# Kernel tuning notes

Hardware: AMD Instinct MI355X
Metric: run time of the kernel (lower is better)

The kernel has to match this reference:

```python
import jax, jax.numpy as jnp
import numpy as np

TOP_K = 8


def setup_inputs() -> dict:
    key = jax.random.key(0)
    k1, k2, k3 = jax.random.split(key, 3)
    N, D, SQRT_K = 8192, 2048, 64
    x = jax.random.normal(k1, (N, D), dtype=jnp.float32)
    W1 = jax.random.normal(k2, (SQRT_K, D), dtype=jnp.float32) * (1.0 / np.sqrt(D))
    W2 = jax.random.normal(k3, (SQRT_K, D), dtype=jnp.float32) * (1.0 / np.sqrt(D))
    return {"x": x, "W1": W1, "W2": W2}


def reference(x, W1, W2):
    # Two small projections: [N, d] @ [d, sqrt_K] -> [N, sqrt_K]
    s1 = jnp.einsum('nd,kd->nk', x, W1)
    s2 = jnp.einsum('nd,kd->nk', x, W2)
    # Outer-sum score matrix: expert (i, j) scores s1[i] + s2[j]; flatten -> [N, sqrt_K^2]
    scores = (s1[:, :, None] + s2[:, None, :]).reshape(x.shape[0], -1)
    topk_vals, topk_idx = jax.lax.top_k(scores, TOP_K)
    probs = jax.nn.softmax(topk_vals, axis=-1)
    return topk_idx, probs, scores
```

## Files before the change

### kernel.cpp

```cpp
#include <hip/hip_runtime.h>
#include <math.h>

#define NROWS 8192
#define DDIM  2048
#define NEXP  4096
#define TK    8
#define KSPLIT 4
#define KRANGE (DDIM / KSPLIT)
#define BM     64

typedef float  f4 __attribute__((ext_vector_type(4)));
typedef double d2 __attribute__((ext_vector_type(2)));

__global__ __launch_bounds__(256, 2) void pkr_gemm64w(const float* __restrict__ x,
                                                      const float* __restrict__ w1,
                                                      const float* __restrict__ w2,
                                                      float* __restrict__ out) {
  __shared__ double xsd[32][66];
  __shared__ double wsd[32][130];

  const int tid   = threadIdx.x;
  const int rb    = blockIdx.x >> 2;
  const int kp    = blockIdx.x & 3;
  const int rows0 = rb * BM;
  const int kbase = kp * KRANGE;

  const int rh = tid >> 4;
  const int ch = tid & 15;

  const int sxr = tid >> 3;
  const int sxk = (tid & 7) * 4;
  const float* xr0 = x + (size_t)(rows0 + sxr) * DDIM + kbase + sxk;
  const float* xr1 = xr0 + (size_t)32 * DDIM;

  const int swc = tid >> 1;
  const int swk = (tid & 1) * 16;
  const float* wr = ((swc < 64) ? (w1 + (size_t)swc * DDIM)
                                : (w2 + (size_t)(swc - 64) * DDIM)) + kbase + swk;

  double acc[4][8] = {};

  for (int cch = 0; cch < KRANGE / 32; ++cch) {
    const int k0 = cch * 32;
    {
      f4 a = *(const f4*)(xr0 + k0);
      f4 b = *(const f4*)(xr1 + k0);
#pragma unroll
      for (int q = 0; q < 4; ++q) {
        xsd[sxk + q][sxr]      = (double)a[q];
        xsd[sxk + q][32 + sxr] = (double)b[q];
      }
    }
#pragma unroll
    for (int p = 0; p < 4; ++p) {
      f4 wv = *(const f4*)(wr + k0 + p * 4);
#pragma unroll
      for (int q = 0; q < 4; ++q)
        wsd[swk + p * 4 + q][swc] = (double)wv[q];
    }
    __syncthreads();

#pragma unroll
    for (int k = 0; k < 32; ++k) {
      const d2 x01 = *(const d2*)&xsd[k][rh * 4];
      const d2 x23 = *(const d2*)&xsd[k][rh * 4 + 2];
      const double xd[4] = { x01[0], x01[1], x23[0], x23[1] };
      d2 wg[4];
#pragma unroll
      for (int g = 0; g < 4; ++g) wg[g] = *(const d2*)&wsd[k][g * 32 + ch * 2];
#pragma unroll
      for (int a = 0; a < 4; ++a)
#pragma unroll
        for (int g = 0; g < 4; ++g) {
          acc[a][2 * g]     += xd[a] * wg[g][0];
          acc[a][2 * g + 1] += xd[a] * wg[g][1];
        }
    }
    __syncthreads();
  }

  double* P = (double*)(out + (size_t)2 * NROWS * TK);
#pragma unroll
  for (int a = 0; a < 4; ++a) {
    double* dst = P + (size_t)(rows0 + rh * 4 + a) * (NEXP / 2) + kp * 128;
#pragma unroll
    for (int g = 0; g < 4; ++g) {
      d2 v; v[0] = acc[a][2 * g]; v[1] = acc[a][2 * g + 1];
      *(d2*)(dst + g * 32 + ch * 2) = v;
    }
  }
}

__device__ __forceinline__ void bitonic64(double& v, int& idx, int lane) {
#pragma unroll
  for (int k = 2; k <= 64; k <<= 1) {
#pragma unroll
    for (int j = k >> 1; j > 0; j >>= 1) {
      const double ov = __shfl_xor(v, j);
      const int    oi = __shfl_xor(idx, j);
      const bool obetter = (ov > v) || (ov == v && oi < idx);
      const bool lower   = (lane & j) == 0;
      const bool up      = (lane & k) == 0;
      if ((lower == up) ? obetter : !obetter) { v = ov; idx = oi; }
    }
  }
}

__global__ __launch_bounds__(256) void pkr_finish(float* __restrict__ out) {
  const int lane = threadIdx.x & 63;
  const int wv   = threadIdx.x >> 6;
  const int row  = blockIdx.x * 4 + wv;

  const double* Pr = (const double*)(out + (size_t)2 * NROWS * TK) + (size_t)row * (NEXP / 2);
  double s1 = 0.0, s2 = 0.0;
#pragma unroll
  for (int p = 0; p < KSPLIT; ++p) {
    s1 += Pr[p * 128 + lane];
    s2 += Pr[p * 128 + 64 + lane];
  }

  __shared__ double sh1[4][64], sh2[4][64];
  sh1[wv][lane] = s1;
  sh2[wv][lane] = s2;
  __syncthreads();

  {
    float* srow = out + (size_t)2 * NROWS * TK + (size_t)row * NEXP;
    const int il = lane >> 4;
    const int jq = (lane & 15) * 4;
    const double sj0 = sh2[wv][jq + 0], sj1 = sh2[wv][jq + 1];
    const double sj2 = sh2[wv][jq + 2], sj3 = sh2[wv][jq + 3];
#pragma unroll
    for (int i0 = 0; i0 < 64; i0 += 4) {
      const double si = sh1[wv][i0 + il];
      f4 v;
      v[0] = (float)(si + sj0);
      v[1] = (float)(si + sj1);
      v[2] = (float)(si + sj2);
      v[3] = (float)(si + sj3);
      *(f4*)(srow + (size_t)(i0 + il) * 64 + jq) = v;
    }
  }

  double v1 = s1; int i1 = lane;
  bitonic64(v1, i1, lane);
  double v2 = s2; int i2 = lane;
  bitonic64(v2, i2, lane);

  const double ca = __shfl(v1, lane >> 3);
  const int    ia = __shfl(i1, lane >> 3);
  const double cb = __shfl(v2, lane & 7);
  const int    ib = __shfl(i2, lane & 7);
  double cv = ca + cb;
  int    ci = ia * 64 + ib;
  bitonic64(cv, ci, lane);

  const double vmax = __shfl(cv, 0);
  float e = expf((float)(cv - vmax));
  float sum = e;
#pragma unroll
  for (int off = 1; off < 8; off <<= 1) sum += __shfl_xor(sum, off);
  if (lane < 8) {
    out[(size_t)row * TK + lane]                      = (float)ci;
    out[(size_t)NROWS * TK + (size_t)row * TK + lane] = e / sum;
  }
}

extern "C" void kernel_launch(void* const* d_in, const int* in_sizes, int n_in,
                              void* d_out, int out_size, void* d_ws, size_t ws_size,
                              hipStream_t stream) {
  const float* x  = (const float*)d_in[0];
  const float* w1 = (const float*)d_in[1];
  const float* w2 = (const float*)d_in[2];
  float* out = (float*)d_out;

  hipLaunchKernelGGL(pkr_gemm64w, dim3((NROWS / BM) * KSPLIT), dim3(256), 0, stream,
                     x, w1, w2, out);
  hipLaunchKernelGGL(pkr_finish, dim3(NROWS / 4), dim3(256), 0, stream, out);
}
```

Measured before the change: 273.9 us.

## Enlarge GEMM tile to 128 rows, prefetch via registers, split top-k into per-thread kernel

The GEMM now covers 128 rows per block with an 8x8 fp64 accumulator per thread. x is staged in LDS as fp32 and converted on read, and the next chunk is prefetched into registers while the current one computes. Top-k selection moves to a separate kernel where each thread handles one row with serial insertion into sorted lists, replacing the wave-level bitonic sorts, and score expansion becomes its own third kernel. This trades more registers, lower occupancy and an extra launch for more data reuse per LDS load, and the top-k kernel launches only 128 blocks of 64 threads.

```diff
diff --git a/kernel.cpp b/kernel.cpp
--- a/kernel.cpp
+++ b/kernel.cpp
@@ -7,17 +7,22 @@
 #define TK    8
 #define KSPLIT 4
 #define KRANGE (DDIM / KSPLIT)
-#define BM     64
+#define BM     128
+#define BK     32
+#define NCH    (KRANGE / BK)
+#define XS     162
+#define WS     162
 
 typedef float  f4 __attribute__((ext_vector_type(4)));
+typedef float  f2 __attribute__((ext_vector_type(2)));
 typedef double d2 __attribute__((ext_vector_type(2)));
 
-__global__ __launch_bounds__(256, 2) void pkr_gemm64w(const float* __restrict__ x,
-                                                      const float* __restrict__ w1,
-                                                      const float* __restrict__ w2,
-                                                      float* __restrict__ out) {
-  __shared__ double xsd[32][66];
-  __shared__ double wsd[32][130];
+__global__ __launch_bounds__(256) void pkr_gemm(const float* __restrict__ x,
+                                                const float* __restrict__ w1,
+                                                const float* __restrict__ w2,
+                                                float* __restrict__ out) {
+  __shared__ float  xs[BK][XS];
+  __shared__ double wsd[BK][WS];
 
   const int tid   = threadIdx.x;
   const int rb    = blockIdx.x >> 2;
@@ -25,88 +30,148 @@
   const int rows0 = rb * BM;
   const int kbase = kp * KRANGE;
 
-  const int rh = tid >> 4;
-  const int ch = tid & 15;
-
-  const int sxr = tid >> 3;
-  const int sxk = (tid & 7) * 4;
-  const float* xr0 = x + (size_t)(rows0 + sxr) * DDIM + kbase + sxk;
-  const float* xr1 = xr0 + (size_t)32 * DDIM;
-
-  const int swc = tid >> 1;
-  const int swk = (tid & 1) * 16;
-  const float* wr = ((swc < 64) ? (w1 + (size_t)swc * DDIM)
-                                : (w2 + (size_t)(swc - 64) * DDIM)) + kbase + swk;
-
-  double acc[4][8] = {};
-
-  for (int cch = 0; cch < KRANGE / 32; ++cch) {
-    const int k0 = cch * 32;
-    {
-      f4 a = *(const f4*)(xr0 + k0);
-      f4 b = *(const f4*)(xr1 + k0);
+  const int tr   = tid >> 4;
+  const int tc   = tid & 15;
+  const int tr10 = tr * 10;
+  const int tc10 = tc * 10;
+
+  int mp[4], mk[4];
+  const float* xp[4];
+  const float* wp[4];
+#pragma unroll
+  for (int i = 0; i < 4; ++i) {
+    const int s  = i * 256 + tid;
+    const int r  = s >> 3;
+    const int kq = (s & 7) * 4;
+    mp[i] = r + (r >> 3) * 2;
+    mk[i] = kq;
+    xp[i] = x + (size_t)(rows0 + r) * DDIM + kbase + kq;
+    wp[i] = ((r < 64) ? (w1 + (size_t)r * DDIM)
+                      : (w2 + (size_t)(r - 64) * DDIM)) + kbase + kq;
+  }
+
+  f4 xfr[4], wfr[4];
+
+  auto load_regs = [&](int ch) {
+    const int o = ch * BK;
+#pragma unroll
+    for (int i = 0; i < 4; ++i) {
+      xfr[i] = *(const f4*)(xp[i] + o);
+      wfr[i] = *(const f4*)(wp[i] + o);
+    }
+  };
+  auto write_lds = [&]() {
+#pragma unroll
+    for (int i = 0; i < 4; ++i)
 #pragma unroll
       for (int q = 0; q < 4; ++q) {
-        xsd[sxk + q][sxr]      = (double)a[q];
-        xsd[sxk + q][32 + sxr] = (double)b[q];
+        xs[mk[i] + q][mp[i]]  = xfr[i][q];
+        wsd[mk[i] + q][mp[i]] = (double)wfr[i][q];
       }
-    }
-#pragma unroll
-    for (int p = 0; p < 4; ++p) {
-      f4 wv = *(const f4*)(wr + k0 + p * 4);
-#pragma unroll
-      for (int q = 0; q < 4; ++q)
-        wsd[swk + p * 4 + q][swc] = (double)wv[q];
+  };
+
+  double acc[8][8] = {};
+
+  load_regs(0);
+  write_lds();
+  __syncthreads();
+
+  for (int ch = 0; ch < NCH; ++ch) {
+    if (ch + 1 < NCH) load_regs(ch + 1);
+#pragma unroll 4
+    for (int k = 0; k < BK; ++k) {
+      double xd[8];
+      d2 wd[4];
+#pragma unroll
+      for (int m = 0; m < 4; ++m) {
+        const f2 xv = *(const f2*)&xs[k][tr10 + 2 * m];
+        xd[2 * m]     = (double)xv[0];
+        xd[2 * m + 1] = (double)xv[1];
+        wd[m] = *(const d2*)&wsd[k][tc10 + 2 * m];
+      }
+#pragma unroll
+      for (int a = 0; a < 8; ++a)
+#pragma unroll
+        for (int m = 0; m < 4; ++m) {
+          acc[a][2 * m]     += xd[a] * wd[m][0];
+          acc[a][2 * m + 1] += xd[a] * wd[m][1];
+        }
     }
     __syncthreads();
-
-#pragma unroll
-    for (int k = 0; k < 32; ++k) {
-      const d2 x01 = *(const d2*)&xsd[k][rh * 4];
-      const d2 x23 = *(const d2*)&xsd[k][rh * 4 + 2];
-      const double xd[4] = { x01[0], x01[1], x23[0], x23[1] };
-      d2 wg[4];
-#pragma unroll
-      for (int g = 0; g < 4; ++g) wg[g] = *(const d2*)&wsd[k][g * 32 + ch * 2];
-#pragma unroll
-      for (int a = 0; a < 4; ++a)
-#pragma unroll
-        for (int g = 0; g < 4; ++g) {
-          acc[a][2 * g]     += xd[a] * wg[g][0];
-          acc[a][2 * g + 1] += xd[a] * wg[g][1];
-        }
-    }
-    __syncthreads();
+    if (ch + 1 < NCH) {
+      write_lds();
+      __syncthreads();
+    }
   }
 
   double* P = (double*)(out + (size_t)2 * NROWS * TK);
 #pragma unroll
-  for (int a = 0; a < 4; ++a) {
-    double* dst = P + (size_t)(rows0 + rh * 4 + a) * (NEXP / 2) + kp * 128;
-#pragma unroll
-    for (int g = 0; g < 4; ++g) {
-      d2 v; v[0] = acc[a][2 * g]; v[1] = acc[a][2 * g + 1];
-      *(d2*)(dst + g * 32 + ch * 2) = v;
-    }
-  }
-}
-
-__device__ __forceinline__ void bitonic64(double& v, int& idx, int lane) {
-#pragma unroll
-  for (int k = 2; k <= 64; k <<= 1) {
-#pragma unroll
-    for (int j = k >> 1; j > 0; j >>= 1) {
-      const double ov = __shfl_xor(v, j);
-      const int    oi = __shfl_xor(idx, j);
-      const bool obetter = (ov > v) || (ov == v && oi < idx);
-      const bool lower   = (lane & j) == 0;
-      const bool up      = (lane & k) == 0;
-      if ((lower == up) ? obetter : !obetter) { v = ov; idx = oi; }
-    }
-  }
-}
-
-__global__ __launch_bounds__(256) void pkr_finish(float* __restrict__ out) {
+  for (int a = 0; a < 8; ++a) {
+    double* dst = P + (size_t)(rows0 + tr * 8 + a) * (NEXP / 2) + kp * 128 + tc * 8;
+#pragma unroll
+    for (int m = 0; m < 4; ++m) {
+      d2 v; v[0] = acc[a][2 * m]; v[1] = acc[a][2 * m + 1];
+      *(d2*)(dst + 2 * m) = v;
+    }
+  }
+}
+
+__device__ __forceinline__ void ins8(double v, int i, double* av, int* ai) {
+  bool b[8];
+#pragma unroll
+  for (int j = 0; j < 8; ++j)
+    b[j] = (v > av[j]) || (v == av[j] && i < ai[j]);
+#pragma unroll
+  for (int j = 7; j > 0; --j) {
+    av[j] = b[j] ? (b[j - 1] ? av[j - 1] : v) : av[j];
+    ai[j] = b[j] ? (b[j - 1] ? ai[j - 1] : i) : ai[j];
+  }
+  if (b[0]) { av[0] = v; ai[0] = i; }
+}
+
+__global__ __launch_bounds__(64) void pkr_topk(float* __restrict__ out) {
+  const int row = blockIdx.x * 64 + threadIdx.x;
+  const double* Pr = (const double*)(out + (size_t)2 * NROWS * TK) + (size_t)row * (NEXP / 2);
+
+  double av[8], bv[8], cv[8];
+  int    ai[8], bi[8], ci[8];
+#pragma unroll
+  for (int t = 0; t < 8; ++t) {
+    av[t] = bv[t] = cv[t] = -INFINITY;
+    ai[t] = bi[t] = ci[t] = 0x7fffffff;
+  }
+
+  for (int j = 0; j < 64; ++j) {
+    const double s = Pr[j] + Pr[128 + j] + Pr[256 + j] + Pr[384 + j];
+    ins8(s, j, av, ai);
+  }
+  for (int j = 0; j < 64; ++j) {
+    const double s = Pr[64 + j] + Pr[192 + j] + Pr[320 + j] + Pr[448 + j];
+    ins8(s, j, bv, bi);
+  }
+#pragma unroll
+  for (int p = 0; p < 8; ++p)
+#pragma unroll
+    for (int q = 0; q < 8; ++q)
+      ins8(av[p] + bv[q], ai[p] * 64 + bi[q], cv, ci);
+
+  float e[8], sum = 0.f;
+#pragma unroll
+  for (int t = 0; t < 8; ++t) { e[t] = expf((float)(cv[t] - cv[0])); sum += e[t]; }
+  const float inv = 1.0f / sum;
+  f4 vi0, vi1, vp0, vp1;
+#pragma unroll
+  for (int t = 0; t < 4; ++t) {
+    vi0[t] = (float)ci[t];     vi1[t] = (float)ci[t + 4];
+    vp0[t] = e[t] * inv;       vp1[t] = e[t + 4] * inv;
+  }
+  float* oi = out + (size_t)row * TK;
+  float* op = out + (size_t)NROWS * TK + (size_t)row * TK;
+  *(f4*)oi = vi0; *(f4*)(oi + 4) = vi1;
+  *(f4*)op = vp0; *(f4*)(op + 4) = vp1;
+}
+
+__global__ __launch_bounds__(256) void pkr_expand(float* __restrict__ out) {
   const int lane = threadIdx.x & 63;
   const int wv   = threadIdx.x >> 6;
   const int row  = blockIdx.x * 4 + wv;
@@ -124,45 +189,20 @@
   sh2[wv][lane] = s2;
   __syncthreads();
 
-  {
-    float* srow = out + (size_t)2 * NROWS * TK + (size_t)row * NEXP;
-    const int il = lane >> 4;
-    const int jq = (lane & 15) * 4;
-    const double sj0 = sh2[wv][jq + 0], sj1 = sh2[wv][jq + 1];
-    const double sj2 = sh2[wv][jq + 2], sj3 = sh2[wv][jq + 3];
-#pragma unroll
-    for (int i0 = 0; i0 < 64; i0 += 4) {
-      const double si = sh1[wv][i0 + il];
-      f4 v;
-      v[0] = (float)(si + sj0);
-      v[1] = (float)(si + sj1);
-      v[2] = (float)(si + sj2);
-      v[3] = (float)(si + sj3);
-      *(f4*)(srow + (size_t)(i0 + il) * 64 + jq) = v;
-    }
-  }
-
-  double v1 = s1; int i1 = lane;
-  bitonic64(v1, i1, lane);
-  double v2 = s2; int i2 = lane;
-  bitonic64(v2, i2, lane);
-
-  const double ca = __shfl(v1, lane >> 3);
-  const int    ia = __shfl(i1, lane >> 3);
-  const double cb = __shfl(v2, lane & 7);
-  const int    ib = __shfl(i2, lane & 7);
-  double cv = ca + cb;
-  int    ci = ia * 64 + ib;
-  bitonic64(cv, ci, lane);
-
-  const double vmax = __shfl(cv, 0);
-  float e = expf((float)(cv - vmax));
-  float sum = e;
-#pragma unroll
-  for (int off = 1; off < 8; off <<= 1) sum += __shfl_xor(sum, off);
-  if (lane < 8) {
-    out[(size_t)row * TK + lane]                      = (float)ci;
-    out[(size_t)NROWS * TK + (size_t)row * TK + lane] = e / sum;
+  float* srow = out + (size_t)2 * NROWS * TK + (size_t)row * NEXP;
+  const int il = lane >> 4;
+  const int jq = (lane & 15) * 4;
+  const double sj0 = sh2[wv][jq + 0], sj1 = sh2[wv][jq + 1];
+  const double sj2 = sh2[wv][jq + 2], sj3 = sh2[wv][jq + 3];
+#pragma unroll
+  for (int i0 = 0; i0 < 64; i0 += 4) {
+    const double si = sh1[wv][i0 + il];
+    f4 v;
+    v[0] = (float)(si + sj0);
+    v[1] = (float)(si + sj1);
+    v[2] = (float)(si + sj2);
+    v[3] = (float)(si + sj3);
+    *(f4*)(srow + (size_t)(i0 + il) * 64 + jq) = v;
   }
 }
 
@@ -174,7 +214,8 @@
   const float* w2 = (const float*)d_in[2];
   float* out = (float*)d_out;
 
-  hipLaunchKernelGGL(pkr_gemm64w, dim3((NROWS / BM) * KSPLIT), dim3(256), 0, stream,
+  hipLaunchKernelGGL(pkr_gemm, dim3((NROWS / BM) * KSPLIT), dim3(256), 0, stream,
                      x, w1, w2, out);
-  hipLaunchKernelGGL(pkr_finish, dim3(NROWS / 4), dim3(256), 0, stream, out);
-}
+  hipLaunchKernelGGL(pkr_topk, dim3(NROWS / 64), dim3(64), 0, stream, out);
+  hipLaunchKernelGGL(pkr_expand, dim3(NROWS / 4), dim3(256), 0, stream, out);
+}
```

Measured after the change: 434.7 us. 58.7% more time.
